# Kernel optimization log

Measured on AMD Instinct MI355X. Metric: run time of the kernel, lower is better.

The kernel has to match this reference:

```python
import jax, jax.numpy as jnp
import numpy as np

B, Q, K, D = 16, 2048, 2048, 512


def setup_inputs() -> dict:
    key = jax.random.key(0)
    kq, kk, kv, kl = jax.random.split(key, 4)
    queries = jax.random.normal(kq, (B, Q, D), dtype=jnp.float32)
    keys = jax.random.normal(kk, (B, K, D), dtype=jnp.float32)
    values = jax.random.normal(kv, (B, K, D), dtype=jnp.float32)
    # lengths in [1, K] so no row is fully masked
    valid_lens = jax.random.randint(kl, (B,), 1, K + 1, dtype=jnp.int32)
    return {"queries": queries, "keys": keys, "values": values, "valid_lens": valid_lens}


def reference(queries, keys, values, valid_lens):
    # scores: [B, Q, K]
    scale = 1.0 / jnp.sqrt(jnp.asarray(queries.shape[-1], queries.dtype))
    scores = jnp.einsum('bqd,bkd->bqk', queries, keys) * scale
    # 1D valid_lens: per-batch key-length mask (positions >= len are masked)
    key_pos = jnp.arange(scores.shape[-1])  # [K]
    mask = key_pos[None, None, :] >= valid_lens[:, None, None]  # [B, 1->Q, K]
    scores = jnp.where(mask, -jnp.inf, scores)
    weights = jax.nn.softmax(scores, axis=-1)  # [B, Q, K]
    # dropout is identity in eval mode (deterministic reference)
    context = jnp.einsum('bqk,bkd->bqd', weights, values)  # [B, Q, D]
    return context, weights
```

## Files before the change

kernel.cpp:

```cpp
#include <hip/hip_runtime.h>
#include <stdint.h>

typedef __bf16 bf16_t;
typedef bf16_t bf16x8 __attribute__((ext_vector_type(8)));
typedef bf16_t bf16x4_t __attribute__((ext_vector_type(4)));
typedef float f32x4 __attribute__((ext_vector_type(4)));

#define NB 16
#define NQ 2048
#define NK 2048
#define ND 512
#define SCALE 0.04419417382415922f

typedef __attribute__((address_space(3))) uint32_t lds_u32;
typedef __attribute__((address_space(1))) const uint32_t glb_u32;

__device__ __forceinline__ float4 ld4(const float* p) { return *(const float4*)p; }

__device__ __forceinline__ f32x4 mfma16(bf16x8 a, bf16x8 b, f32x4 c) {
  return __builtin_amdgcn_mfma_f32_16x16x32_bf16(a, b, c, 0, 0, 0);
}

__global__ __launch_bounds__(256) void qkprep_kernel(const float* __restrict__ Qf,
                                                     const float* __restrict__ Kf,
                                                     bf16_t* __restrict__ Qb,
                                                     bf16_t* __restrict__ Kb) {
  int x = blockIdx.x;
  int b = blockIdx.y;
  const float* src = blockIdx.z ? Kf : Qf;
  bf16_t* dst = blockIdx.z ? Kb : Qb;
  int rt = x >> 4, kt = x & 15;
  const float* s = src + ((size_t)b * 2048 + (size_t)rt * 128) * 512 + kt * 32;
  bf16_t* dtile = dst + (((size_t)b * 16 + rt) * 16 + kt) * 4096;
  int t = threadIdx.x;
#pragma unroll
  for (int i = 0; i < 2; ++i) {
    int d = i * 256 + t;
    int r = d >> 2, slot = d & 3;
    int c = slot ^ ((r >> 1) & 3);
    const float* p = s + (size_t)r * 512 + c * 8;
    float4 v0 = ld4(p), v1 = ld4(p + 4);
    bf16x8 o;
    o[0] = (bf16_t)v0.x; o[1] = (bf16_t)v0.y; o[2] = (bf16_t)v0.z; o[3] = (bf16_t)v0.w;
    o[4] = (bf16_t)v1.x; o[5] = (bf16_t)v1.y; o[6] = (bf16_t)v1.z; o[7] = (bf16_t)v1.w;
    *(bf16x8*)(dtile + (size_t)d * 8) = o;
  }
}

__global__ __launch_bounds__(256) void vt_kernel(const float* __restrict__ V,
                                                 bf16_t* __restrict__ VT,
                                                 const int* __restrict__ lens) {
  int kb = blockIdx.x, b = blockIdx.y;
  if (kb * 32 >= lens[b]) return;
  const float* vsrc = V + ((size_t)b * NK + kb * 32) * ND;
  bf16_t* dst = VT + ((size_t)(b * 64 + kb)) * (512 * 32);
  __shared__ alignas(16) bf16_t Ls[32][128];
  int t = threadIdx.x;
  for (int dbase = 0; dbase < ND; dbase += 128) {
#pragma unroll
    for (int i = 0; i < 4; ++i) {
      int p = i * 256 + t;
      int k = p >> 5, c4 = p & 31;
      float4 v = ld4(vsrc + (size_t)k * ND + dbase + c4 * 4);
      union { bf16_t h[4]; uint2 u; } pk;
      pk.h[0] = (bf16_t)v.x; pk.h[1] = (bf16_t)v.y;
      pk.h[2] = (bf16_t)v.z; pk.h[3] = (bf16_t)v.w;
      *(uint2*)(&Ls[k][c4 * 4]) = pk.u;
    }
    __syncthreads();
    int d = dbase + (t >> 1);
    int h = t & 1;
    int sr = d >> 1;
#pragma unroll
    for (int gg = 0; gg < 2; ++gg) {
      int g = h * 2 + gg;
      bf16x8 v;
#pragma unroll
      for (int j = 0; j < 8; ++j) v[j] = Ls[g * 8 + j][d - dbase];
      int slot = (((d & 1) << 2) | g) ^ (sr & 7);
      *(bf16x8*)(dst + ((size_t)sr * 8 + slot) * 8) = v;
    }
    __syncthreads();
  }
}

__global__ __launch_bounds__(256, 3) void qk_kernel(const bf16_t* __restrict__ Qb,
                                                    const bf16_t* __restrict__ Kb,
                                                    float* __restrict__ P,
                                                    float* __restrict__ psum,
                                                    const int* __restrict__ lens) {
  int bid = blockIdx.x;
  int swz = (bid & 7) * 512 + (bid >> 3);
  int b = swz >> 8;
  int tile = swz & 255;
  int qt = tile >> 4, nt = tile & 15;

  int len = lens[b];
  int q0 = qt * 128;
  int col0 = nt * 128;
  if (col0 >= len) return;

  __shared__ alignas(16) bf16_t As[2][4096];
  __shared__ alignas(16) bf16_t Bs[2][4096];
  __shared__ float rsm[128];

  int t = threadIdx.x;
  int lane = t & 63;
  int wid = t >> 6;
  int wm = wid >> 1, wn = wid & 1;
  int l15 = lane & 15, l4 = lane >> 4;

  float* prow = P + ((size_t)b * NQ + q0) * NK;
  const bf16_t* qtile = Qb + (((size_t)b * 16 + qt) * 16) * 4096;
  const bf16_t* ktile = Kb + (((size_t)b * 16 + nt) * 16) * 4096;

  f32x4 acc[4][4];
  f32x4 zz = {0.f, 0.f, 0.f, 0.f};
#pragma unroll
  for (int mi = 0; mi < 4; ++mi)
#pragma unroll
    for (int ni = 0; ni < 4; ++ni) acc[mi][ni] = zz;

  int eo = wid * 512 + lane * 8;

  auto stage = [&](int kt, int buf) {
    const bf16_t* qa = qtile + (size_t)kt * 4096;
    const bf16_t* ka = ktile + (size_t)kt * 4096;
    bf16_t* la = &As[buf][0];
    bf16_t* lb = &Bs[buf][0];
#pragma unroll
    for (int j = 0; j < 2; ++j) {
      __builtin_amdgcn_global_load_lds((glb_u32*)(qa + j * 2048 + eo),
                                       (lds_u32*)(la + j * 2048 + wid * 512), 16, 0, 0);
      __builtin_amdgcn_global_load_lds((glb_u32*)(ka + j * 2048 + eo),
                                       (lds_u32*)(lb + j * 2048 + wid * 512), 16, 0, 0);
    }
  };

  auto compute = [&](int buf) {
    bf16x8 af[4], bv[4];
#pragma unroll
    for (int mi = 0; mi < 4; ++mi) {
      int row = wm * 64 + mi * 16 + l15;
      int ch = row * 4 + (l4 ^ ((row >> 1) & 3));
      af[mi] = *(const bf16x8*)(&As[buf][ch * 8]);
    }
#pragma unroll
    for (int ni = 0; ni < 4; ++ni) {
      int row = wn * 64 + ni * 16 + l15;
      int ch = row * 4 + (l4 ^ ((row >> 1) & 3));
      bv[ni] = *(const bf16x8*)(&Bs[buf][ch * 8]);
    }
#pragma unroll
    for (int mi = 0; mi < 4; ++mi)
#pragma unroll
      for (int ni = 0; ni < 4; ++ni)
        acc[mi][ni] = mfma16(af[mi], bv[ni], acc[mi][ni]);
  };

  stage(0, 0);
  __syncthreads();
#pragma unroll 1
  for (int kt = 0; kt < 16; ++kt) {
    if (kt + 1 < 16) stage(kt + 1, (kt + 1) & 1);
    compute(kt & 1);
    __syncthreads();
  }

  float rsum[4][4];
#pragma unroll
  for (int mi = 0; mi < 4; ++mi)
#pragma unroll
    for (int r = 0; r < 4; ++r) rsum[mi][r] = 0.f;

#pragma unroll
  for (int mi = 0; mi < 4; ++mi) {
#pragma unroll
    for (int ni = 0; ni < 4; ++ni) {
      int col = col0 + wn * 64 + ni * 16 + l15;
      bool valid = col < len;
#pragma unroll
      for (int r = 0; r < 4; ++r) {
        float e = valid ? __expf(acc[mi][ni][r] * SCALE) : 0.f;
        bf16_t eb = (bf16_t)e;
        rsum[mi][r] += (float)eb;
        bf16_t* purow =
            (bf16_t*)(prow + (size_t)(wm * 64 + mi * 16 + l4 * 4 + r) * NK) + 2048;
        purow[col] = eb;
      }
    }
  }

#pragma unroll
  for (int off = 1; off < 16; off <<= 1)
#pragma unroll
    for (int mi = 0; mi < 4; ++mi)
#pragma unroll
      for (int r = 0; r < 4; ++r)
        rsum[mi][r] += __shfl_xor(rsum[mi][r], off, 64);

  if (wn == 0 && l15 == 0) {
#pragma unroll
    for (int mi = 0; mi < 4; ++mi)
#pragma unroll
      for (int r = 0; r < 4; ++r)
        rsm[wm * 64 + mi * 16 + l4 * 4 + r] = rsum[mi][r];
  }
  __syncthreads();
  if (wn == 1 && l15 == 0) {
#pragma unroll
    for (int mi = 0; mi < 4; ++mi)
#pragma unroll
      for (int r = 0; r < 4; ++r) {
        int row = wm * 64 + mi * 16 + l4 * 4 + r;
        psum[((size_t)b * 16 + nt) * NQ + q0 + row] = rsum[mi][r] + rsm[row];
      }
  }
}

__global__ __launch_bounds__(512, 2) void pv_kernel(float* __restrict__ P,
                                                    const bf16_t* __restrict__ VT,
                                                    float* __restrict__ ctx,
                                                    const float* __restrict__ psum,
                                                    const int* __restrict__ lens) {
  int qt = blockIdx.x, b = blockIdx.y;
  int q0 = qt * 64;
  int len = lens[b];
  int nsteps = (len + 31) >> 5;
  int nvalid = (len + 127) >> 7;

  __shared__ alignas(16) bf16_t Ps[2][64 * 32];
  __shared__ alignas(16) bf16_t Vs[2][512 * 32];
  __shared__ float rcp[64];

  int t = threadIdx.x;
  if (t < 64) {
    float s = 0.f;
    for (int i = 0; i < nvalid; ++i) s += psum[((size_t)b * 16 + i) * NQ + q0 + t];
    rcp[t] = 1.0f / s;
  }
  __syncthreads();

  float* prow = P + ((size_t)b * NQ + q0) * NK;
  const bf16_t* vtb = VT + ((size_t)b * 64) * (512 * 32);

  int lane = t & 63, wid = t >> 6;
  int l15 = lane & 15, l4 = lane >> 4;

  f32x4 acc[4][4];
  f32x4 zz = {0.f, 0.f, 0.f, 0.f};
#pragma unroll
  for (int mi = 0; mi < 4; ++mi)
#pragma unroll
    for (int ni = 0; ni < 4; ++ni) acc[mi][ni] = zz;

  int srow = t >> 3, sc4 = t & 7;
  float rr = rcp[srow];
  const bf16_t* purow = (const bf16_t*)(prow + (size_t)srow * NK) + 2048;

  bf16x4_t pld;
  bf16x8 vld[4];

  auto stage_load = [&](int ks) {
    pld = *(const bf16x4_t*)(purow + ks * 32 + sc4 * 4);
    const bf16_t* src = vtb + (size_t)ks * (512 * 32);
#pragma unroll
    for (int i = 0; i < 4; ++i)
      vld[i] = *(const bf16x8*)(src + ((size_t)i * 512 + t) * 8);
  };
  auto stage_finish = [&](int ks, int buf) {
    float4 w;
    w.x = (float)pld[0] * rr; w.y = (float)pld[1] * rr;
    w.z = (float)pld[2] * rr; w.w = (float)pld[3] * rr;
    *(float4*)(prow + (size_t)srow * NK + ks * 32 + sc4 * 4) = w;
    int sr = srow >> 1;
    int slot = (((srow & 1) << 2) | (sc4 >> 1)) ^ (sr & 7);
    union { bf16_t h[4]; uint2 u; } pk;
    pk.h[0] = (bf16_t)w.x; pk.h[1] = (bf16_t)w.y;
    pk.h[2] = (bf16_t)w.z; pk.h[3] = (bf16_t)w.w;
    *(uint2*)(&Ps[buf][((size_t)sr * 8 + slot) * 8 + (sc4 & 1) * 4]) = pk.u;
#pragma unroll
    for (int i = 0; i < 4; ++i)
      *(bf16x8*)(&Vs[buf][((size_t)i * 512 + t) * 8]) = vld[i];
  };
  auto compute = [&](int cur) {
    bf16x8 af[4], bv[4];
#pragma unroll
    for (int mi = 0; mi < 4; ++mi) {
      int row = mi * 16 + l15;
      af[mi] = *(const bf16x8*)(&Ps[cur][((row >> 1) * 8 + ((((row & 1) << 2) | l4) ^ ((row >> 1) & 7))) * 8]);
    }
#pragma unroll
    for (int ni = 0; ni < 4; ++ni) {
      int d = wid * 64 + ni * 16 + l15;
      bv[ni] = *(const bf16x8*)(&Vs[cur][((d >> 1) * 8 + ((((d & 1) << 2) | l4) ^ ((d >> 1) & 7))) * 8]);
    }
#pragma unroll
    for (int mi = 0; mi < 4; ++mi)
#pragma unroll
      for (int ni = 0; ni < 4; ++ni)
        acc[mi][ni] = mfma16(af[mi], bv[ni], acc[mi][ni]);
  };

  stage_load(0);
  stage_finish(0, 0);
  __syncthreads();
  for (int ks = 0; ks < nsteps; ++ks) {
    int cur = ks & 1;
    if (ks + 1 < nsteps) stage_load(ks + 1);
    compute(cur);
    if (ks == 62 && nsteps == 64) __syncthreads();
    if (ks + 1 < nsteps) stage_finish(ks + 1, cur ^ 1);
    __syncthreads();
  }

  {
    float4 z = make_float4(0.f, 0.f, 0.f, 0.f);
    int tr = t >> 3, tc = t & 7;
    for (int c = nsteps * 32 + tc * 4; c < NK; c += 32)
      *(float4*)(prow + (size_t)tr * NK + c) = z;
  }

  float* crow = ctx + ((size_t)b * NQ + q0) * ND + wid * 64;
#pragma unroll
  for (int mi = 0; mi < 4; ++mi)
#pragma unroll
    for (int ni = 0; ni < 4; ++ni)
#pragma unroll
      for (int r = 0; r < 4; ++r)
        crow[(size_t)(mi * 16 + l4 * 4 + r) * ND + ni * 16 + l15] = acc[mi][ni][r];
}

extern "C" void kernel_launch(void* const* d_in, const int* in_sizes, int n_in,
                              void* d_out, int out_size, void* d_ws, size_t ws_size,
                              hipStream_t stream) {
  const float* Q = (const float*)d_in[0];
  const float* K = (const float*)d_in[1];
  const float* V = (const float*)d_in[2];
  const int* lens = (const int*)d_in[3];

  float* ctx = (float*)d_out;
  float* P = ctx + (size_t)NB * NQ * ND;

  float* psum = (float*)d_ws;
  char* base = (char*)d_ws + (size_t)NB * 16 * NQ * sizeof(float);
  bf16_t* Qb = (bf16_t*)base;
  bf16_t* Kb = (bf16_t*)(base + (size_t)NB * NQ * ND * 2);
  bf16_t* VT = (bf16_t*)(base + (size_t)2 * NB * NQ * ND * 2);

  qkprep_kernel<<<dim3(256, 16, 2), 256, 0, stream>>>(Q, K, Qb, Kb);
  vt_kernel<<<dim3(64, 16), 256, 0, stream>>>(V, VT, lens);
  qk_kernel<<<dim3(4096), 256, 0, stream>>>(Qb, Kb, P, psum, lens);
  pv_kernel<<<dim3(32, 16), 512, 0, stream>>>(P, VT, ctx, psum, lens);
}
```

Baseline: 310.8 us.

## Fuse V transpose into prep kernel and read V fragments directly from global in PV

Merges the V transpose/convert kernel into the Q/K prep kernel as a third grid slice, split across four blocks per key chunk, which removes one launch and adds parallelism. In the PV kernel the V tile no longer goes through LDS: each wave loads its MFMA B fragments straight from the pre-swizzled global VT buffer. This frees the large Vs shared array, so launch bounds rise to 4 blocks per CU. The grid is also flattened with the batch index varying fastest. The trade is that V fragments now come from L2/global inside the compute step instead of from prefetched LDS, which can expose load latency.

```diff
diff --git a/kernel.cpp b/kernel.cpp
--- a/kernel.cpp
+++ b/kernel.cpp
@@ -21,18 +21,55 @@
   return __builtin_amdgcn_mfma_f32_16x16x32_bf16(a, b, c, 0, 0, 0);
 }
 
-__global__ __launch_bounds__(256) void qkprep_kernel(const float* __restrict__ Qf,
-                                                     const float* __restrict__ Kf,
-                                                     bf16_t* __restrict__ Qb,
-                                                     bf16_t* __restrict__ Kb) {
+__global__ __launch_bounds__(256) void prep_kernel(const float* __restrict__ Qf,
+                                                   const float* __restrict__ Kf,
+                                                   const float* __restrict__ Vf,
+                                                   bf16_t* __restrict__ Qb,
+                                                   bf16_t* __restrict__ Kb,
+                                                   bf16_t* __restrict__ VT,
+                                                   const int* __restrict__ lens) {
   int x = blockIdx.x;
   int b = blockIdx.y;
-  const float* src = blockIdx.z ? Kf : Qf;
-  bf16_t* dst = blockIdx.z ? Kb : Qb;
+  int z = blockIdx.z;
+  int t = threadIdx.x;
+
+  if (z == 2) {
+    int kb = x >> 2, dq = (x & 3) * 128;
+    if (kb * 32 >= lens[b]) return;
+    const float* vsrc = Vf + ((size_t)b * NK + kb * 32) * ND;
+    bf16_t* dst = VT + ((size_t)(b * 64 + kb)) * (512 * 32);
+    __shared__ alignas(16) bf16_t Ls[32][128];
+#pragma unroll
+    for (int i = 0; i < 4; ++i) {
+      int p = i * 256 + t;
+      int k = p >> 5, c4 = p & 31;
+      float4 v = ld4(vsrc + (size_t)k * ND + dq + c4 * 4);
+      union { bf16_t h[4]; uint2 u; } pk;
+      pk.h[0] = (bf16_t)v.x; pk.h[1] = (bf16_t)v.y;
+      pk.h[2] = (bf16_t)v.z; pk.h[3] = (bf16_t)v.w;
+      *(uint2*)(&Ls[k][c4 * 4]) = pk.u;
+    }
+    __syncthreads();
+    int d = dq + (t >> 1);
+    int h = t & 1;
+    int sr = d >> 1;
+#pragma unroll
+    for (int gg = 0; gg < 2; ++gg) {
+      int g = h * 2 + gg;
+      bf16x8 v;
+#pragma unroll
+      for (int j = 0; j < 8; ++j) v[j] = Ls[g * 8 + j][d - dq];
+      int slot = (((d & 1) << 2) | g) ^ (sr & 7);
+      *(bf16x8*)(dst + ((size_t)sr * 8 + slot) * 8) = v;
+    }
+    return;
+  }
+
+  const float* src = z ? Kf : Qf;
+  bf16_t* dst = z ? Kb : Qb;
   int rt = x >> 4, kt = x & 15;
   const float* s = src + ((size_t)b * 2048 + (size_t)rt * 128) * 512 + kt * 32;
   bf16_t* dtile = dst + (((size_t)b * 16 + rt) * 16 + kt) * 4096;
-  int t = threadIdx.x;
 #pragma unroll
   for (int i = 0; i < 2; ++i) {
     int d = i * 256 + t;
@@ -47,43 +84,6 @@
   }
 }
 
-__global__ __launch_bounds__(256) void vt_kernel(const float* __restrict__ V,
-                                                 bf16_t* __restrict__ VT,
-                                                 const int* __restrict__ lens) {
-  int kb = blockIdx.x, b = blockIdx.y;
-  if (kb * 32 >= lens[b]) return;
-  const float* vsrc = V + ((size_t)b * NK + kb * 32) * ND;
-  bf16_t* dst = VT + ((size_t)(b * 64 + kb)) * (512 * 32);
-  __shared__ alignas(16) bf16_t Ls[32][128];
-  int t = threadIdx.x;
-  for (int dbase = 0; dbase < ND; dbase += 128) {
-#pragma unroll
-    for (int i = 0; i < 4; ++i) {
-      int p = i * 256 + t;
-      int k = p >> 5, c4 = p & 31;
-      float4 v = ld4(vsrc + (size_t)k * ND + dbase + c4 * 4);
-      union { bf16_t h[4]; uint2 u; } pk;
-      pk.h[0] = (bf16_t)v.x; pk.h[1] = (bf16_t)v.y;
-      pk.h[2] = (bf16_t)v.z; pk.h[3] = (bf16_t)v.w;
-      *(uint2*)(&Ls[k][c4 * 4]) = pk.u;
-    }
-    __syncthreads();
-    int d = dbase + (t >> 1);
-    int h = t & 1;
-    int sr = d >> 1;
-#pragma unroll
-    for (int gg = 0; gg < 2; ++gg) {
-      int g = h * 2 + gg;
-      bf16x8 v;
-#pragma unroll
-      for (int j = 0; j < 8; ++j) v[j] = Ls[g * 8 + j][d - dbase];
-      int slot = (((d & 1) << 2) | g) ^ (sr & 7);
-      *(bf16x8*)(dst + ((size_t)sr * 8 + slot) * 8) = v;
-    }
-    __syncthreads();
-  }
-}
-
 __global__ __launch_bounds__(256, 3) void qk_kernel(const bf16_t* __restrict__ Qb,
                                                     const bf16_t* __restrict__ Kb,
                                                     float* __restrict__ P,
@@ -123,9 +123,9 @@
 
   int eo = wid * 512 + lane * 8;
 
-  auto stage = [&](int kt, int buf) {
-    const bf16_t* qa = qtile + (size_t)kt * 4096;
-    const bf16_t* ka = ktile + (size_t)kt * 4096;
+  auto stage = [&](int kt2, int buf) {
+    const bf16_t* qa = qtile + (size_t)kt2 * 4096;
+    const bf16_t* ka = ktile + (size_t)kt2 * 4096;
     bf16_t* la = &As[buf][0];
     bf16_t* lb = &Bs[buf][0];
 #pragma unroll
@@ -161,9 +161,9 @@
   stage(0, 0);
   __syncthreads();
 #pragma unroll 1
-  for (int kt = 0; kt < 16; ++kt) {
-    if (kt + 1 < 16) stage(kt + 1, (kt + 1) & 1);
-    compute(kt & 1);
+  for (int kt2 = 0; kt2 < 16; ++kt2) {
+    if (kt2 + 1 < 16) stage(kt2 + 1, (kt2 + 1) & 1);
+    compute(kt2 & 1);
     __syncthreads();
   }
 
@@ -218,19 +218,19 @@
   }
 }
 
-__global__ __launch_bounds__(512, 2) void pv_kernel(float* __restrict__ P,
+__global__ __launch_bounds__(512, 4) void pv_kernel(float* __restrict__ P,
                                                     const bf16_t* __restrict__ VT,
                                                     float* __restrict__ ctx,
                                                     const float* __restrict__ psum,
                                                     const int* __restrict__ lens) {
-  int qt = blockIdx.x, b = blockIdx.y;
+  int bid = blockIdx.x;
+  int b = bid & 15, qt = bid >> 4;
   int q0 = qt * 64;
   int len = lens[b];
   int nsteps = (len + 31) >> 5;
   int nvalid = (len + 127) >> 7;
 
   __shared__ alignas(16) bf16_t Ps[2][64 * 32];
-  __shared__ alignas(16) bf16_t Vs[2][512 * 32];
   __shared__ float rcp[64];
 
   int t = threadIdx.x;
@@ -258,15 +258,17 @@
   float rr = rcp[srow];
   const bf16_t* purow = (const bf16_t*)(prow + (size_t)srow * NK) + 2048;
 
+  int vchunk[4];
+#pragma unroll
+  for (int ni = 0; ni < 4; ++ni) {
+    int d = wid * 64 + ni * 16 + l15;
+    vchunk[ni] = ((d >> 1) * 8 + ((((d & 1) << 2) | l4) ^ ((d >> 1) & 7))) * 8;
+  }
+
   bf16x4_t pld;
-  bf16x8 vld[4];
 
   auto stage_load = [&](int ks) {
     pld = *(const bf16x4_t*)(purow + ks * 32 + sc4 * 4);
-    const bf16_t* src = vtb + (size_t)ks * (512 * 32);
-#pragma unroll
-    for (int i = 0; i < 4; ++i)
-      vld[i] = *(const bf16x8*)(src + ((size_t)i * 512 + t) * 8);
   };
   auto stage_finish = [&](int ks, int buf) {
     float4 w;
@@ -279,23 +281,20 @@
     pk.h[0] = (bf16_t)w.x; pk.h[1] = (bf16_t)w.y;
     pk.h[2] = (bf16_t)w.z; pk.h[3] = (bf16_t)w.w;
     *(uint2*)(&Ps[buf][((size_t)sr * 8 + slot) * 8 + (sc4 & 1) * 4]) = pk.u;
-#pragma unroll
-    for (int i = 0; i < 4; ++i)
-      *(bf16x8*)(&Vs[buf][((size_t)i * 512 + t) * 8]) = vld[i];
-  };
-  auto compute = [&](int cur) {
-    bf16x8 af[4], bv[4];
+  };
+  auto compute = [&](int ks, int cur) {
+    const bf16_t* vsrc = vtb + (size_t)ks * (512 * 32);
+    bf16x8 bv[4];
+#pragma unroll
+    for (int ni = 0; ni < 4; ++ni)
+      bv[ni] = *(const bf16x8*)(vsrc + vchunk[ni]);
+    bf16x8 af[4];
 #pragma unroll
     for (int mi = 0; mi < 4; ++mi) {
       int row = mi * 16 + l15;
       af[mi] = *(const bf16x8*)(&Ps[cur][((row >> 1) * 8 + ((((row & 1) << 2) | l4) ^ ((row >> 1) & 7))) * 8]);
     }
 #pragma unroll
-    for (int ni = 0; ni < 4; ++ni) {
-      int d = wid * 64 + ni * 16 + l15;
-      bv[ni] = *(const bf16x8*)(&Vs[cur][((d >> 1) * 8 + ((((d & 1) << 2) | l4) ^ ((d >> 1) & 7))) * 8]);
-    }
-#pragma unroll
     for (int mi = 0; mi < 4; ++mi)
 #pragma unroll
       for (int ni = 0; ni < 4; ++ni)
@@ -305,20 +304,19 @@
   stage_load(0);
   stage_finish(0, 0);
   __syncthreads();
+#pragma unroll 1
   for (int ks = 0; ks < nsteps; ++ks) {
     int cur = ks & 1;
     if (ks + 1 < nsteps) stage_load(ks + 1);
-    compute(cur);
-    if (ks == 62 && nsteps == 64) __syncthreads();
+    compute(ks, cur);
     if (ks + 1 < nsteps) stage_finish(ks + 1, cur ^ 1);
     __syncthreads();
   }
 
   {
     float4 z = make_float4(0.f, 0.f, 0.f, 0.f);
-    int tr = t >> 3, tc = t & 7;
-    for (int c = nsteps * 32 + tc * 4; c < NK; c += 32)
-      *(float4*)(prow + (size_t)tr * NK + c) = z;
+    for (int c = nsteps * 32 + sc4 * 4; c < NK; c += 32)
+      *(float4*)(prow + (size_t)srow * NK + c) = z;
   }
 
   float* crow = ctx + ((size_t)b * NQ + q0) * ND + wid * 64;
@@ -348,8 +346,7 @@
   bf16_t* Kb = (bf16_t*)(base + (size_t)NB * NQ * ND * 2);
   bf16_t* VT = (bf16_t*)(base + (size_t)2 * NB * NQ * ND * 2);
 
-  qkprep_kernel<<<dim3(256, 16, 2), 256, 0, stream>>>(Q, K, Qb, Kb);
-  vt_kernel<<<dim3(64, 16), 256, 0, stream>>>(V, VT, lens);
+  prep_kernel<<<dim3(256, 16, 3), 256, 0, stream>>>(Q, K, V, Qb, Kb, VT, lens);
   qk_kernel<<<dim3(4096), 256, 0, stream>>>(Qb, Kb, P, psum, lens);
-  pv_kernel<<<dim3(32, 16), 512, 0, stream>>>(P, VT, ctx, psum, lens);
-}
+  pv_kernel<<<dim3(512), 512, 0, stream>>>(P, VT, ctx, psum, lens);
+}
```

After: 284.1 us. 8.6% less time.
